# Optimization experiments

Hardware: AMD Instinct MI355X
Metric: run time of the kernel (lower is better)

Reference implementation:

```python
import jax, jax.numpy as jnp
import numpy as np

B_, L_, D_, H_ = 2, 1024, 1024, 16


def _matrixR(L, d_model):
    # Transformer-XL sinusoid table, reversed along the position axis (reverse=True)
    inv_freq = 1.0 / (10000.0 ** (np.arange(0, d_model, 2, dtype=np.float32) / d_model))
    sinus = np.arange(L, dtype=np.float32)[:, None] * inv_freq[None, :]
    mat = np.zeros((L, d_model), dtype=np.float32)
    mat[:, 0::2] = np.sin(sinus)
    mat[:, 1::2] = np.cos(sinus)
    return jnp.asarray(mat[::-1].copy())


def _shift_b(x):
    # x: (b, h, L, L) -> TXL relative shift + lower-triangular mask
    b, h, L, _ = x.shape
    pad = jnp.concatenate([jnp.zeros((b, h, L, 1), x.dtype), x], axis=-1)  # (b,h,L,L+1)
    shifted = pad.reshape(b, h, L + 1, L)[:, :, 1:, :]                      # (b,h,L,L)
    return jnp.tril(shifted)


def setup_inputs() -> dict:
    key = jax.random.key(0)
    ks = jax.random.split(key, 8)
    s = 1.0 / np.sqrt(D_)
    return {
        "E": jax.random.normal(ks[0], (B_, L_, D_), dtype=jnp.float32),
        "Ev": jax.random.normal(ks[1], (B_, L_, D_), dtype=jnp.float32),
        "R": _matrixR(L_, D_),
        "Wq": jax.random.normal(ks[2], (D_, D_), dtype=jnp.float32) * s,
        "Wke": jax.random.normal(ks[3], (D_, D_), dtype=jnp.float32) * s,
        "Wkr": jax.random.normal(ks[4], (D_, D_), dtype=jnp.float32) * s,
        "Wv": jax.random.normal(ks[5], (D_, D_), dtype=jnp.float32) * s,
        "cb": jnp.ones((D_,), dtype=jnp.float32),
        "pb": jnp.ones((D_,), dtype=jnp.float32),
        "Wo_w": jax.random.normal(ks[6], (D_, D_), dtype=jnp.float32) * s,
        "Wo_b": jnp.zeros((D_,), dtype=jnp.float32),
        "ln_g": jnp.ones((D_,), dtype=jnp.float32),
        "ln_b": jnp.zeros((D_,), dtype=jnp.float32),
    }


def reference(E, Ev, R, Wq, Wke, Wkr, Wv, cb, pb, Wo_w, Wo_b, ln_g, ln_b):
    b, L, d = E.shape
    h = H_
    dh = d // h
    # projections -> (b, h, L, dh)
    q = (E @ Wq).reshape(b, L, h, dh).transpose(0, 2, 1, 3)
    k = (Ev @ Wke).reshape(b, L, h, dh).transpose(0, 2, 1, 3)
    v = (Ev @ Wv).reshape(b, L, h, dh).transpose(0, 2, 1, 3)
    # relative-position keys (batch independent): (h, L, dh)
    Q = (R @ Wkr).reshape(L, h, dh).transpose(1, 0, 2)
    # (a) content-content
    A_a = jnp.einsum('bhid,bhjd->bhij', q, k)
    # (b) content-position, with shift trick
    A_b = _shift_b(jnp.einsum('bhid,hjd->bhij', q, Q))
    # (c) global content bias (same for every query row)
    A_c = jnp.einsum('hd,bhjd->bhj', cb.reshape(h, dh), k)[:, :, None, :]  # (b,h,1,L)
    # (d) global position bias (batch independent), shifted
    d_row = jnp.einsum('hd,hjd->hj', pb.reshape(h, dh), Q)                 # (h,L)
    A_d = _shift_b(jnp.broadcast_to(d_row[None, :, None, :], (1, h, L, L)))
    A = A_a + A_b + A_c + A_d
    p = jax.nn.softmax(A, axis=-1)
    Oh = jnp.einsum('bhij,bhjd->bhid', p, v)
    O = Oh.transpose(0, 2, 1, 3).reshape(b, L, d)
    # residual + output proj (dropout is identity in eval) + LayerNorm
    res = Ev + (O @ Wo_w + Wo_b)
    mu = jnp.mean(res, axis=-1, keepdims=True)
    var = jnp.mean((res - mu) ** 2, axis=-1, keepdims=True)
    return (res - mu) * jax.lax.rsqrt(var + 1e-5) * ln_g + ln_b
```

## Files before the change

### kernel.cpp

```cpp
#include <hip/hip_runtime.h>
#include <hip/hip_bf16.h>
#include <math.h>

#define B_ 2
#define L_ 1024
#define D_ 1024
#define H_ 16

typedef short short8 __attribute__((ext_vector_type(8)));
typedef float f32x4  __attribute__((ext_vector_type(4)));

__device__ __forceinline__ short f2bf(float f) {
  unsigned u = __float_as_uint(f);
  u += 0x7fff + ((u >> 16) & 1);
  return (short)(u >> 16);
}
__device__ __forceinline__ float bf2f(short s) {
  return __uint_as_float(((unsigned)(unsigned short)s) << 16);
}
__device__ __forceinline__ int swz(int row, int slot) {
  return row * 64 + ((slot ^ (row & 7)) << 3);
}
__device__ __forceinline__ int vswz(int d, int j) {
  return d * 64 + ((((j >> 3) ^ (d & 7) ^ ((d >> 3) & 7)) & 7) << 3) + (j & 7);
}

__device__ __forceinline__ void glds16(const void* g, void* l) {
  __builtin_amdgcn_global_load_lds((const __attribute__((address_space(1))) void*)g,
                                   (__attribute__((address_space(3))) void*)l, 16, 0, 0);
}

__global__ __launch_bounds__(256) void castbf(
    const float* __restrict__ E, const float* __restrict__ Ev,
    const float* __restrict__ R, short* __restrict__ o) {
  size_t i8 = ((size_t)blockIdx.x * 256 + threadIdx.x) * 8;
  const float* src; size_t off;
  if (i8 < 2097152)      { src = E;  off = i8; }
  else if (i8 < 4194304) { src = Ev; off = i8 - 2097152; }
  else                   { src = R;  off = i8 - 4194304; }
  float4 a = *(const float4*)&src[off];
  float4 b = *(const float4*)&src[off + 4];
  short8 v;
  v[0] = f2bf(a.x); v[1] = f2bf(a.y); v[2] = f2bf(a.z); v[3] = f2bf(a.w);
  v[4] = f2bf(b.x); v[5] = f2bf(b.y); v[6] = f2bf(b.z); v[7] = f2bf(b.w);
  *(short8*)&o[i8] = v;
}

template<int OUT_F32>
__device__ __forceinline__ void mm_glds(const short* __restrict__ A,
                                        const short* __restrict__ Bt,
                                        void* Cp, int N, int K,
                                        int bx, int by) {
  __shared__ short As[8192];
  __shared__ short Bs[8192];
  const int tid = threadIdx.x;
  const int l = tid & 63, w = tid >> 6;
  const int row0 = by * 128, col0 = bx * 128;
  const int wm = (w >> 1) * 64, wn = (w & 1) * 64;
  const f32x4 fz = {0.f, 0.f, 0.f, 0.f};

  f32x4 acc[4][4];
  #pragma unroll
  for (int i = 0; i < 4; ++i)
    #pragma unroll
    for (int j = 0; j < 4; ++j) acc[i][j] = fz;

  const int lrow = l >> 3;
  const int lcol = (l & 7) * 8;

  for (int t = 0; t < K / 64; ++t) {
    const int k0 = t * 64;
    if (t) __syncthreads();
    #pragma unroll
    for (int c = 0; c < 4; ++c) {
      const int rr = (w * 4 + c) * 8 + lrow;
      glds16(&A[(size_t)(row0 + rr) * K + k0 + lcol], &As[(w * 4 + c) * 512]);
      glds16(&Bt[(size_t)(col0 + rr) * K + k0 + lcol], &Bs[(w * 4 + c) * 512]);
    }
    __syncthreads();
    #pragma unroll
    for (int kf = 0; kf < 2; ++kf) {
      short8 a[4], b[4];
      #pragma unroll
      for (int mf = 0; mf < 4; ++mf)
        a[mf] = *(const short8*)&As[(wm + mf * 16 + (l & 15)) * 64 + (kf * 4 + (l >> 4)) * 8];
      #pragma unroll
      for (int nf = 0; nf < 4; ++nf)
        b[nf] = *(const short8*)&Bs[(wn + nf * 16 + (l & 15)) * 64 + (kf * 4 + (l >> 4)) * 8];
      #pragma unroll
      for (int mf = 0; mf < 4; ++mf)
        #pragma unroll
        for (int nf = 0; nf < 4; ++nf)
          acc[mf][nf] = __builtin_amdgcn_mfma_f32_16x16x32_bf16(a[mf], b[nf], acc[mf][nf], 0, 0, 0);
    }
  }

  #pragma unroll
  for (int mf = 0; mf < 4; ++mf)
    #pragma unroll
    for (int nf = 0; nf < 4; ++nf)
      #pragma unroll
      for (int r = 0; r < 4; ++r) {
        int row = row0 + wm + mf * 16 + (l >> 4) * 4 + r;
        int col = col0 + wn + nf * 16 + (l & 15);
        if (OUT_F32) ((float*)Cp)[(size_t)row * N + col] = acc[mf][nf][r];
        else         ((short*)Cp)[(size_t)row * N + col] = f2bf(acc[mf][nf][r]);
      }
}

__global__ __launch_bounds__(256) void proj_mfma(
    const short* __restrict__ Eb, const short* __restrict__ Evb,
    const short* __restrict__ Rb, const short* __restrict__ Wt,
    short* __restrict__ qb, short* __restrict__ kb,
    short* __restrict__ vb, short* __restrict__ Qpb) {
  const int z = blockIdx.z;
  const short* A; const short* Bt; short* C; int M;
  const size_t MM = (size_t)D_ * D_;
  if (z == 0)      { A = Eb;  Bt = Wt;          C = qb;  M = B_ * L_; }
  else if (z == 1) { A = Evb; Bt = Wt + MM;     C = kb;  M = B_ * L_; }
  else if (z == 2) { A = Evb; Bt = Wt + 3 * MM; C = vb;  M = B_ * L_; }
  else             { A = Rb;  Bt = Wt + 2 * MM; C = Qpb; M = L_;      }
  if ((int)blockIdx.y * 128 >= M) return;
  mm_glds<0>(A, Bt, C, D_, D_, blockIdx.x, blockIdx.y);
}

__global__ __launch_bounds__(256) void out_mfma(
    const short* __restrict__ Ob, const short* __restrict__ Wot, float* __restrict__ proj) {
  mm_glds<1>(Ob, Wot, proj, D_, D_, blockIdx.x, blockIdx.y);
}

__global__ __launch_bounds__(256) void tcast(
    const float* __restrict__ W0, const float* __restrict__ W1,
    const float* __restrict__ W2, const float* __restrict__ W3,
    const float* __restrict__ W4, short* __restrict__ out) {
  const int z = blockIdx.z;
  const float* W = (z == 0) ? W0 : (z == 1) ? W1 : (z == 2) ? W2 : (z == 3) ? W3 : W4;
  short* Wt = out + (size_t)z * D_ * D_;
  __shared__ short t[64][65];
  const int tid = threadIdx.x;
  const int r0 = blockIdx.y * 64, c0 = blockIdx.x * 64;
  #pragma unroll
  for (int i = 0; i < 4; ++i) {
    int idx = tid + i * 256;
    int r = idx >> 4, c4 = (idx & 15) * 4;
    float4 v = *(const float4*)&W[(size_t)(r0 + r) * D_ + c0 + c4];
    t[c4 + 0][r] = f2bf(v.x); t[c4 + 1][r] = f2bf(v.y);
    t[c4 + 2][r] = f2bf(v.z); t[c4 + 3][r] = f2bf(v.w);
  }
  __syncthreads();
  #pragma unroll
  for (int i = 0; i < 2; ++i) {
    int idx = tid + i * 256;
    int rr = idx >> 3, cc = (idx & 7) * 8;
    short8 o;
    #pragma unroll
    for (int e = 0; e < 8; ++e) o[e] = t[rr][cc + e];
    *(short8*)&Wt[(size_t)(c0 + rr) * D_ + r0 + cc] = o;
  }
}

__global__ __launch_bounds__(256) void cdvec(
    const short* __restrict__ kb, const short* __restrict__ Qpb,
    const float* __restrict__ cb, const float* __restrict__ pb,
    float* __restrict__ cvec, float* __restrict__ dvec) {
  int idx = blockIdx.x * 256 + threadIdx.x;
  if (idx < B_ * H_ * L_) {
    int b = idx >> 14, h = (idx >> 10) & 15, j = idx & 1023;
    const short* kr = &kb[(size_t)(b * L_ + j) * D_ + h * 64];
    const float* cr = &cb[h * 64];
    float s = 0.f;
    #pragma unroll
    for (int d8 = 0; d8 < 8; ++d8) {
      short8 kv = *(const short8*)&kr[d8 * 8];
      #pragma unroll
      for (int e = 0; e < 8; ++e) s += bf2f(kv[e]) * cr[d8 * 8 + e];
    }
    cvec[idx] = s;
  } else {
    int i2 = idx - B_ * H_ * L_;
    if (i2 < H_ * L_) {
      int h = i2 >> 10, m = i2 & 1023;
      const short* qr = &Qpb[(size_t)m * D_ + h * 64];
      const float* pr = &pb[h * 64];
      float s = 0.f;
      #pragma unroll
      for (int d8 = 0; d8 < 8; ++d8) {
        short8 qv = *(const short8*)&qr[d8 * 8];
        #pragma unroll
        for (int e = 0; e < 8; ++e) s += bf2f(qv[e]) * pr[d8 * 8 + e];
      }
      dvec[i2] = s;
    }
  }
}

__global__ __launch_bounds__(256) void attn_mfma(
    const short* __restrict__ qb, const short* __restrict__ kb,
    const short* __restrict__ vb, const short* __restrict__ Qpb,
    const float* __restrict__ cvec, const float* __restrict__ dvec,
    short* __restrict__ Ob) {
  __shared__ short q_s[4096];
  __shared__ short k_s[4096];
  __shared__ short vt_s[4096];
  __shared__ short win_s[8192];
  __shared__ short pb_s[4 * 1312];
  __shared__ float cvec_s[64];
  __shared__ float dvec_s[128];

  const int tid = threadIdx.x;
  const int l = tid & 63, w = tid >> 6;
  const int nib = L_ / 64;
  const int b  = blockIdx.x / (H_ * nib);
  const int hh = (blockIdx.x / nib) % H_;
  const int i0 = (blockIdx.x % nib) * 64;
  const f32x4 fz = {0.f, 0.f, 0.f, 0.f};
  const short8 sz = {0, 0, 0, 0, 0, 0, 0, 0};

  short8 rk[2], rv[2], rw[4];
  float rc = 0.f, rd = 0.f;

  auto stage_load = [&](int jt) {
    const int j0 = jt * 64;
    const bool pos = (j0 <= i0);
    const int mbase = L_ - 64 - i0 + j0;
    #pragma unroll
    for (int c = 0; c < 2; ++c) {
      int ci = tid + c * 256;
      int r = ci >> 3, s = ci & 7;
      rk[c] = *(const short8*)&kb[(size_t)(b * L_ + j0 + r) * D_ + hh * 64 + s * 8];
      rv[c] = *(const short8*)&vb[(size_t)(b * L_ + j0 + r) * D_ + hh * 64 + s * 8];
    }
    if (pos) {
      #pragma unroll
      for (int c = 0; c < 4; ++c) {
        int ci = tid + c * 256;
        int mm = ci >> 3, s = ci & 7;
        int m = mbase + mm;
        rw[c] = (m < L_) ? *(const short8*)&Qpb[(size_t)m * D_ + hh * 64 + s * 8] : sz;
      }
      if (tid < 128) {
        int m = mbase + tid;
        rd = (m < L_) ? dvec[hh * L_ + m] : 0.f;
      }
    }
    if (tid < 64) rc = cvec[(size_t)(b * H_ + hh) * L_ + j0 + tid];
  };

  auto stage_write = [&](int jt) {
    const bool pos = (jt * 64 <= i0);
    #pragma unroll
    for (int c = 0; c < 2; ++c) {
      int ci = tid + c * 256;
      int r = ci >> 3, s = ci & 7;
      *(short8*)&k_s[swz(r, s)] = rk[c];
      #pragma unroll
      for (int e = 0; e < 8; ++e) {
        int d = s * 8 + e;
        vt_s[vswz(d, r)] = rv[c][e];
      }
    }
    if (pos) {
      #pragma unroll
      for (int c = 0; c < 4; ++c) {
        int ci = tid + c * 256;
        int mm = ci >> 3, s = ci & 7;
        *(short8*)&win_s[swz(mm, s)] = rw[c];
      }
      if (tid < 128) dvec_s[tid] = rd;
    }
    if (tid < 64) cvec_s[tid] = rc;
  };

  short8 rq[2];
  #pragma unroll
  for (int c = 0; c < 2; ++c) {
    int ci = tid + c * 256;
    int r = ci >> 3, s = ci & 7;
    rq[c] = *(const short8*)&qb[(size_t)(b * L_ + i0 + r) * D_ + hh * 64 + s * 8];
  }
  stage_load(0);
  #pragma unroll
  for (int c = 0; c < 2; ++c) {
    int ci = tid + c * 256;
    *(short8*)&q_s[swz(ci >> 3, ci & 7)] = rq[c];
  }
  __syncthreads();

  short8 aq[2];
  {
    int row = w * 16 + (l & 15);
    aq[0] = *(const short8*)&q_s[swz(row, (l >> 4))];
    aq[1] = *(const short8*)&q_s[swz(row, 4 + (l >> 4))];
  }

  float mrow[4], lrow[4];
  f32x4 oacc[4];
  #pragma unroll
  for (int r = 0; r < 4; ++r) { mrow[r] = -3.0e38f; lrow[r] = 0.f; }
  #pragma unroll
  for (int nf = 0; nf < 4; ++nf) oacc[nf] = fz;

  for (int jt = 0; jt < 16; ++jt) {
    const int j0 = jt * 64;
    const bool pos = (j0 <= i0);
    const bool diag = (j0 == i0);

    stage_write(jt);
    __syncthreads();
    if (jt < 15) stage_load(jt + 1);

    f32x4 sac[4];
    #pragma unroll
    for (int nf = 0; nf < 4; ++nf) sac[nf] = fz;
    #pragma unroll
    for (int kf = 0; kf < 2; ++kf) {
      #pragma unroll
      for (int nf = 0; nf < 4; ++nf) {
        short8 bk = *(const short8*)&k_s[swz(nf * 16 + (l & 15), kf * 4 + (l >> 4))];
        sac[nf] = __builtin_amdgcn_mfma_f32_16x16x32_bf16(aq[kf], bk, sac[nf], 0, 0, 0);
      }
    }

    if (pos) {
      f32x4 pacc[5];
      #pragma unroll
      for (int u = 0; u < 5; ++u) pacc[u] = fz;
      const int nf0 = 3 - w;
      #pragma unroll
      for (int kf = 0; kf < 2; ++kf) {
        #pragma unroll
        for (int u = 0; u < 5; ++u) {
          short8 bw = *(const short8*)&win_s[swz((nf0 + u) * 16 + (l & 15), kf * 4 + (l >> 4))];
          pacc[u] = __builtin_amdgcn_mfma_f32_16x16x32_bf16(aq[kf], bw, pacc[u], 0, 0, 0);
        }
      }
      const int pbb = w * 1312;
      #pragma unroll
      for (int u = 0; u < 5; ++u)
        #pragma unroll
        for (int r = 0; r < 4; ++r) {
          int row = (l >> 4) * 4 + r;
          pb_s[pbb + row * 82 + u * 16 + (l & 15)] = f2bf(pacc[u][r]);
        }
    }

    #pragma unroll
    for (int nf = 0; nf < 4; ++nf)
      #pragma unroll
      for (int r = 0; r < 4; ++r) {
        int rj = nf * 16 + (l & 15);
        float s = sac[nf][r] + cvec_s[rj];
        if (pos) {
          int ris = (l >> 4) * 4 + r;
          int rib = w * 16 + ris;
          if (!diag || rj <= rib) {
            s += bf2f(pb_s[w * 1312 + ris * 82 + (15 - ris + rj)]);
            s += dvec_s[63 - rib + rj];
          }
        }
        sac[nf][r] = s;
      }

    #pragma unroll
    for (int r = 0; r < 4; ++r) {
      float mx = fmaxf(fmaxf(sac[0][r], sac[1][r]), fmaxf(sac[2][r], sac[3][r]));
      #pragma unroll
      for (int off = 1; off < 16; off <<= 1)
        mx = fmaxf(mx, __shfl_xor(mx, off, 64));
      float mn = fmaxf(mrow[r], mx);
      float sc = __expf(mrow[r] - mn);
      mrow[r] = mn;
      float ls = 0.f;
      #pragma unroll
      for (int nf = 0; nf < 4; ++nf) {
        float p = __expf(sac[nf][r] - mn);
        sac[nf][r] = p;
        ls += p;
      }
      #pragma unroll
      for (int off = 1; off < 16; off <<= 1)
        ls += __shfl_xor(ls, off, 64);
      lrow[r] = lrow[r] * sc + ls;
      #pragma unroll
      for (int nf = 0; nf < 4; ++nf) oacc[nf][r] *= sc;
    }

    #pragma unroll
    for (int nf = 0; nf < 4; ++nf)
      #pragma unroll
      for (int r = 0; r < 4; ++r) {
        int row = (l >> 4) * 4 + r;
        int col = nf * 16 + (l & 15);
        pb_s[w * 1312 + row * 64 + (((col >> 3) ^ (row & 7)) << 3) + (col & 7)] = f2bf(sac[nf][r]);
      }

    #pragma unroll
    for (int kf = 0; kf < 2; ++kf) {
      int prow = l & 15;
      short8 ap = *(const short8*)&pb_s[w * 1312 + prow * 64 + (((kf * 4 + (l >> 4)) ^ (prow & 7)) << 3)];
      #pragma unroll
      for (int nf = 0; nf < 4; ++nf) {
        short8 bv = *(const short8*)&vt_s[vswz(nf * 16 + (l & 15), (kf * 4 + (l >> 4)) * 8)];
        oacc[nf] = __builtin_amdgcn_mfma_f32_16x16x32_bf16(ap, bv, oacc[nf], 0, 0, 0);
      }
    }
    __syncthreads();
  }

  #pragma unroll
  for (int r = 0; r < 4; ++r) {
    float inv = 1.f / lrow[r];
    #pragma unroll
    for (int nf = 0; nf < 4; ++nf) {
      int row = i0 + w * 16 + (l >> 4) * 4 + r;
      int col = hh * 64 + nf * 16 + (l & 15);
      Ob[(size_t)(b * L_ + row) * D_ + col] = f2bf(oacc[nf][r] * inv);
    }
  }
}

__global__ __launch_bounds__(256) void ln_kernel(
    const float* __restrict__ Ev, const float* __restrict__ proj,
    const float* __restrict__ Wo_b, const float* __restrict__ g,
    const float* __restrict__ beta, float* __restrict__ out) {
  const int row = blockIdx.x;
  __shared__ float red[8];
  const int tid = threadIdx.x;
  const int d = tid * 4;

  float4 e  = *(const float4*)&Ev[(size_t)row * D_ + d];
  float4 p  = *(const float4*)&proj[(size_t)row * D_ + d];
  float4 wb = *(const float4*)&Wo_b[d];
  float4 rr = { e.x + p.x + wb.x, e.y + p.y + wb.y,
                e.z + p.z + wb.z, e.w + p.w + wb.w };
  float sum = rr.x + rr.y + rr.z + rr.w;
  float sq  = rr.x * rr.x + rr.y * rr.y + rr.z * rr.z + rr.w * rr.w;

  #pragma unroll
  for (int off = 1; off < 64; off <<= 1) {
    sum += __shfl_xor(sum, off, 64);
    sq  += __shfl_xor(sq,  off, 64);
  }
  const int wid = tid >> 6;
  if ((tid & 63) == 0) { red[wid * 2] = sum; red[wid * 2 + 1] = sq; }
  __syncthreads();
  sum = red[0] + red[2] + red[4] + red[6];
  sq  = red[1] + red[3] + red[5] + red[7];

  const float mu   = sum * (1.f / (float)D_);
  const float var  = sq * (1.f / (float)D_) - mu * mu;
  const float rstd = rsqrtf(var + 1e-5f);

  float4 gg = *(const float4*)&g[d];
  float4 bb = *(const float4*)&beta[d];
  float4 o = { (rr.x - mu) * rstd * gg.x + bb.x,
               (rr.y - mu) * rstd * gg.y + bb.y,
               (rr.z - mu) * rstd * gg.z + bb.z,
               (rr.w - mu) * rstd * gg.w + bb.w };
  *(float4*)&out[(size_t)row * D_ + d] = o;
}

extern "C" void kernel_launch(void* const* d_in, const int* in_sizes, int n_in,
                              void* d_out, int out_size, void* d_ws, size_t ws_size,
                              hipStream_t stream) {
  const float* E    = (const float*)d_in[0];
  const float* Ev   = (const float*)d_in[1];
  const float* R    = (const float*)d_in[2];
  const float* Wq   = (const float*)d_in[3];
  const float* Wke  = (const float*)d_in[4];
  const float* Wkr  = (const float*)d_in[5];
  const float* Wv   = (const float*)d_in[6];
  const float* cb   = (const float*)d_in[7];
  const float* pb   = (const float*)d_in[8];
  const float* Wo_w = (const float*)d_in[9];
  const float* Wo_b = (const float*)d_in[10];
  const float* ln_g = (const float*)d_in[11];
  const float* ln_b = (const float*)d_in[12];
  float* out = (float*)d_out;

  short* ws   = (short*)d_ws;
  short* Eb   = ws;
  short* Evb  = ws + 2097152;
  short* Rb   = ws + 4194304;
  short* qb   = ws + 5242880;
  short* kb   = ws + 7340032;
  short* vb   = ws + 9437184;
  short* Qpb  = ws + 11534336;
  short* Wt   = ws + 12582912;
  short* Ob   = ws + 17825792;
  float* proj = (float*)Eb;
  float* cvec = (float*)Rb;
  float* dvec = cvec + 32768;

  castbf<<<2560, 256, 0, stream>>>(E, Ev, R, Eb);

  tcast<<<dim3(16, 16, 5), 256, 0, stream>>>(Wq, Wke, Wkr, Wv, Wo_w, Wt);

  proj_mfma<<<dim3(8, 16, 4), 256, 0, stream>>>(Eb, Evb, Rb, Wt, qb, kb, vb, Qpb);

  cdvec<<<192, 256, 0, stream>>>(kb, Qpb, cb, pb, cvec, dvec);

  attn_mfma<<<B_ * H_ * (L_ / 64), 256, 0, stream>>>(qb, kb, vb, Qpb, cvec, dvec, Ob);

  out_mfma<<<dim3(8, 16), 256, 0, stream>>>(Ob, Wt + 4 * (size_t)D_ * D_, proj);

  ln_kernel<<<B_ * L_, 256, 0, stream>>>(Ev, proj, Wo_b, ln_g, ln_b, out);
}
```

Before: 227.0 us.

## Split attention over key halves with combine pass, retile GEMMs, fuse prep kernels

Attention is split into two key-range halves along a second grid dimension. Each half writes unnormalized fp32 partial outputs plus its running max and sum, and a new combine kernel merges the halves into the bf16 output. This doubles the number of attention blocks so more CUs stay busy. The projection and output GEMMs move from 128x128 to 64-row tiles (128 or 64 columns) with an XOR-swizzled LDS layout, giving more blocks and fewer bank conflicts. The activation cast and weight transpose-cast kernels are merged into one launch. MFMA sections are wrapped in s_setprio, and the P-tile swizzle key changes. The cost is an extra kernel plus fp32 partial-output traffic through reused workspace.

```diff
diff --git a/kernel.cpp b/kernel.cpp
--- a/kernel.cpp
+++ b/kernel.cpp
@@ -19,10 +19,13 @@
   return __uint_as_float(((unsigned)(unsigned short)s) << 16);
 }
 __device__ __forceinline__ int swz(int row, int slot) {
-  return row * 64 + ((slot ^ (row & 7)) << 3);
+  return row * 64 + (((slot ^ row) & 7) << 3);
 }
 __device__ __forceinline__ int vswz(int d, int j) {
   return d * 64 + ((((j >> 3) ^ (d & 7) ^ ((d >> 3) & 7)) & 7) << 3) + (j & 7);
+}
+__device__ __forceinline__ int pkey(int row) {
+  return (row & 7) ^ ((row & 8) >> 2);
 }
 
 __device__ __forceinline__ void glds16(const void* g, void* l) {
@@ -30,75 +33,113 @@
                                    (__attribute__((address_space(3))) void*)l, 16, 0, 0);
 }
 
-__global__ __launch_bounds__(256) void castbf(
+__global__ __launch_bounds__(256) void prep(
     const float* __restrict__ E, const float* __restrict__ Ev,
-    const float* __restrict__ R, short* __restrict__ o) {
-  size_t i8 = ((size_t)blockIdx.x * 256 + threadIdx.x) * 8;
-  const float* src; size_t off;
-  if (i8 < 2097152)      { src = E;  off = i8; }
-  else if (i8 < 4194304) { src = Ev; off = i8 - 2097152; }
-  else                   { src = R;  off = i8 - 4194304; }
-  float4 a = *(const float4*)&src[off];
-  float4 b = *(const float4*)&src[off + 4];
-  short8 v;
-  v[0] = f2bf(a.x); v[1] = f2bf(a.y); v[2] = f2bf(a.z); v[3] = f2bf(a.w);
-  v[4] = f2bf(b.x); v[5] = f2bf(b.y); v[6] = f2bf(b.z); v[7] = f2bf(b.w);
-  *(short8*)&o[i8] = v;
-}
-
-template<int OUT_F32>
-__device__ __forceinline__ void mm_glds(const short* __restrict__ A,
-                                        const short* __restrict__ Bt,
-                                        void* Cp, int N, int K,
-                                        int bx, int by) {
-  __shared__ short As[8192];
-  __shared__ short Bs[8192];
+    const float* __restrict__ R,
+    const float* __restrict__ W0, const float* __restrict__ W1,
+    const float* __restrict__ W2, const float* __restrict__ W3,
+    const float* __restrict__ W4,
+    short* __restrict__ act, short* __restrict__ Wt) {
+  __shared__ short t[64][65];
+  const int tid = threadIdx.x;
+  int bid = blockIdx.x;
+  if (bid < 2560) {
+    size_t i8 = ((size_t)bid * 256 + tid) * 8;
+    const float* src; size_t off;
+    if (i8 < 2097152)      { src = E;  off = i8; }
+    else if (i8 < 4194304) { src = Ev; off = i8 - 2097152; }
+    else                   { src = R;  off = i8 - 4194304; }
+    float4 a = *(const float4*)&src[off];
+    float4 b = *(const float4*)&src[off + 4];
+    short8 v;
+    v[0] = f2bf(a.x); v[1] = f2bf(a.y); v[2] = f2bf(a.z); v[3] = f2bf(a.w);
+    v[4] = f2bf(b.x); v[5] = f2bf(b.y); v[6] = f2bf(b.z); v[7] = f2bf(b.w);
+    *(short8*)&act[i8] = v;
+    return;
+  }
+  bid -= 2560;
+  const int z = bid >> 8, rem = bid & 255;
+  const int by = rem >> 4, bx = rem & 15;
+  const float* W = (z == 0) ? W0 : (z == 1) ? W1 : (z == 2) ? W2 : (z == 3) ? W3 : W4;
+  short* Wtz = Wt + (size_t)z * D_ * D_;
+  const int r0 = by * 64, c0 = bx * 64;
+  #pragma unroll
+  for (int i = 0; i < 4; ++i) {
+    int idx = tid + i * 256;
+    int r = idx >> 4, c4 = (idx & 15) * 4;
+    float4 v = *(const float4*)&W[(size_t)(r0 + r) * D_ + c0 + c4];
+    t[c4 + 0][r] = f2bf(v.x); t[c4 + 1][r] = f2bf(v.y);
+    t[c4 + 2][r] = f2bf(v.z); t[c4 + 3][r] = f2bf(v.w);
+  }
+  __syncthreads();
+  #pragma unroll
+  for (int i = 0; i < 2; ++i) {
+    int idx = tid + i * 256;
+    int rr = idx >> 3, cc = (idx & 7) * 8;
+    short8 o;
+    #pragma unroll
+    for (int e = 0; e < 8; ++e) o[e] = t[rr][cc + e];
+    *(short8*)&Wtz[(size_t)(c0 + rr) * D_ + r0 + cc] = o;
+  }
+}
+
+template<int NF, int OUT_F32>
+__device__ __forceinline__ void mm_nf(const short* __restrict__ A,
+                                      const short* __restrict__ Bt,
+                                      void* Cp, int N, int K, int bx, int by) {
+  constexpr int BN = NF * 32;
+  __shared__ short As[4096];
+  __shared__ short Bs[BN * 64];
   const int tid = threadIdx.x;
   const int l = tid & 63, w = tid >> 6;
-  const int row0 = by * 128, col0 = bx * 128;
-  const int wm = (w >> 1) * 64, wn = (w & 1) * 64;
+  const int row0 = by * 64, col0 = bx * BN;
+  const int wm = (w >> 1) * 32, wn = (w & 1) * (NF * 16);
+  const int lr = l >> 3;
+  const int lc = ((l & 7) ^ lr) * 8;
   const f32x4 fz = {0.f, 0.f, 0.f, 0.f};
 
-  f32x4 acc[4][4];
-  #pragma unroll
-  for (int i = 0; i < 4; ++i)
-    #pragma unroll
-    for (int j = 0; j < 4; ++j) acc[i][j] = fz;
-
-  const int lrow = l >> 3;
-  const int lcol = (l & 7) * 8;
+  f32x4 acc[2][NF];
+  #pragma unroll
+  for (int i = 0; i < 2; ++i)
+    #pragma unroll
+    for (int j = 0; j < NF; ++j) acc[i][j] = fz;
 
   for (int t = 0; t < K / 64; ++t) {
     const int k0 = t * 64;
     if (t) __syncthreads();
     #pragma unroll
-    for (int c = 0; c < 4; ++c) {
-      const int rr = (w * 4 + c) * 8 + lrow;
-      glds16(&A[(size_t)(row0 + rr) * K + k0 + lcol], &As[(w * 4 + c) * 512]);
-      glds16(&Bt[(size_t)(col0 + rr) * K + k0 + lcol], &Bs[(w * 4 + c) * 512]);
+    for (int c = 0; c < 2; ++c) {
+      int ch = w * 2 + c;
+      glds16(&A[(size_t)(row0 + ch * 8 + lr) * K + k0 + lc], &As[ch * 512]);
+    }
+    #pragma unroll
+    for (int c = 0; c < NF; ++c) {
+      int ch = w * NF + c;
+      glds16(&Bt[(size_t)(col0 + ch * 8 + lr) * K + k0 + lc], &Bs[ch * 512]);
     }
     __syncthreads();
     #pragma unroll
     for (int kf = 0; kf < 2; ++kf) {
-      short8 a[4], b[4];
-      #pragma unroll
-      for (int mf = 0; mf < 4; ++mf)
-        a[mf] = *(const short8*)&As[(wm + mf * 16 + (l & 15)) * 64 + (kf * 4 + (l >> 4)) * 8];
-      #pragma unroll
-      for (int nf = 0; nf < 4; ++nf)
-        b[nf] = *(const short8*)&Bs[(wn + nf * 16 + (l & 15)) * 64 + (kf * 4 + (l >> 4)) * 8];
-      #pragma unroll
-      for (int mf = 0; mf < 4; ++mf)
+      const int slot = kf * 4 + (l >> 4);
+      short8 a[2], b[NF];
+      #pragma unroll
+      for (int mf = 0; mf < 2; ++mf)
+        a[mf] = *(const short8*)&As[swz(wm + mf * 16 + (l & 15), slot)];
+      #pragma unroll
+      for (int nf = 0; nf < NF; ++nf)
+        b[nf] = *(const short8*)&Bs[swz(wn + nf * 16 + (l & 15), slot)];
+      #pragma unroll
+      for (int mf = 0; mf < 2; ++mf)
         #pragma unroll
-        for (int nf = 0; nf < 4; ++nf)
+        for (int nf = 0; nf < NF; ++nf)
           acc[mf][nf] = __builtin_amdgcn_mfma_f32_16x16x32_bf16(a[mf], b[nf], acc[mf][nf], 0, 0, 0);
     }
   }
 
   #pragma unroll
-  for (int mf = 0; mf < 4; ++mf)
-    #pragma unroll
-    for (int nf = 0; nf < 4; ++nf)
+  for (int mf = 0; mf < 2; ++mf)
+    #pragma unroll
+    for (int nf = 0; nf < NF; ++nf)
       #pragma unroll
       for (int r = 0; r < 4; ++r) {
         int row = row0 + wm + mf * 16 + (l >> 4) * 4 + r;
@@ -120,43 +161,13 @@
   else if (z == 1) { A = Evb; Bt = Wt + MM;     C = kb;  M = B_ * L_; }
   else if (z == 2) { A = Evb; Bt = Wt + 3 * MM; C = vb;  M = B_ * L_; }
   else             { A = Rb;  Bt = Wt + 2 * MM; C = Qpb; M = L_;      }
-  if ((int)blockIdx.y * 128 >= M) return;
-  mm_glds<0>(A, Bt, C, D_, D_, blockIdx.x, blockIdx.y);
+  if ((int)blockIdx.y * 64 >= M) return;
+  mm_nf<4, 0>(A, Bt, C, D_, D_, blockIdx.x, blockIdx.y);
 }
 
 __global__ __launch_bounds__(256) void out_mfma(
     const short* __restrict__ Ob, const short* __restrict__ Wot, float* __restrict__ proj) {
-  mm_glds<1>(Ob, Wot, proj, D_, D_, blockIdx.x, blockIdx.y);
-}
-
-__global__ __launch_bounds__(256) void tcast(
-    const float* __restrict__ W0, const float* __restrict__ W1,
-    const float* __restrict__ W2, const float* __restrict__ W3,
-    const float* __restrict__ W4, short* __restrict__ out) {
-  const int z = blockIdx.z;
-  const float* W = (z == 0) ? W0 : (z == 1) ? W1 : (z == 2) ? W2 : (z == 3) ? W3 : W4;
-  short* Wt = out + (size_t)z * D_ * D_;
-  __shared__ short t[64][65];
-  const int tid = threadIdx.x;
-  const int r0 = blockIdx.y * 64, c0 = blockIdx.x * 64;
-  #pragma unroll
-  for (int i = 0; i < 4; ++i) {
-    int idx = tid + i * 256;
-    int r = idx >> 4, c4 = (idx & 15) * 4;
-    float4 v = *(const float4*)&W[(size_t)(r0 + r) * D_ + c0 + c4];
-    t[c4 + 0][r] = f2bf(v.x); t[c4 + 1][r] = f2bf(v.y);
-    t[c4 + 2][r] = f2bf(v.z); t[c4 + 3][r] = f2bf(v.w);
-  }
-  __syncthreads();
-  #pragma unroll
-  for (int i = 0; i < 2; ++i) {
-    int idx = tid + i * 256;
-    int rr = idx >> 3, cc = (idx & 7) * 8;
-    short8 o;
-    #pragma unroll
-    for (int e = 0; e < 8; ++e) o[e] = t[rr][cc + e];
-    *(short8*)&Wt[(size_t)(c0 + rr) * D_ + r0 + cc] = o;
-  }
+  mm_nf<2, 1>(Ob, Wot, proj, D_, D_, blockIdx.x, blockIdx.y);
 }
 
 __global__ __launch_bounds__(256) void cdvec(
@@ -198,12 +209,11 @@
     const short* __restrict__ qb, const short* __restrict__ kb,
     const short* __restrict__ vb, const short* __restrict__ Qpb,
     const float* __restrict__ cvec, const float* __restrict__ dvec,
-    short* __restrict__ Ob) {
-  __shared__ short q_s[4096];
+    float* __restrict__ O0, float* __restrict__ O1, float* __restrict__ ml) {
   __shared__ short k_s[4096];
   __shared__ short vt_s[4096];
   __shared__ short win_s[8192];
-  __shared__ short pb_s[4 * 1312];
+  __shared__ short pbq_s[5248];
   __shared__ float cvec_s[64];
   __shared__ float dvec_s[128];
 
@@ -213,6 +223,8 @@
   const int b  = blockIdx.x / (H_ * nib);
   const int hh = (blockIdx.x / nib) % H_;
   const int i0 = (blockIdx.x % nib) * 64;
+  const int split = blockIdx.y;
+  const int jt0 = split * 8, jt1 = jt0 + 8;
   const f32x4 fz = {0.f, 0.f, 0.f, 0.f};
   const short8 sz = {0, 0, 0, 0, 0, 0, 0, 0};
 
@@ -275,22 +287,21 @@
   #pragma unroll
   for (int c = 0; c < 2; ++c) {
     int ci = tid + c * 256;
-    int r = ci >> 3, s = ci & 7;
-    rq[c] = *(const short8*)&qb[(size_t)(b * L_ + i0 + r) * D_ + hh * 64 + s * 8];
-  }
-  stage_load(0);
+    rq[c] = *(const short8*)&qb[(size_t)(b * L_ + i0 + (ci >> 3)) * D_ + hh * 64 + (ci & 7) * 8];
+  }
+  stage_load(jt0);
   #pragma unroll
   for (int c = 0; c < 2; ++c) {
     int ci = tid + c * 256;
-    *(short8*)&q_s[swz(ci >> 3, ci & 7)] = rq[c];
+    *(short8*)&pbq_s[swz(ci >> 3, ci & 7)] = rq[c];
   }
   __syncthreads();
 
   short8 aq[2];
   {
     int row = w * 16 + (l & 15);
-    aq[0] = *(const short8*)&q_s[swz(row, (l >> 4))];
-    aq[1] = *(const short8*)&q_s[swz(row, 4 + (l >> 4))];
+    aq[0] = *(const short8*)&pbq_s[swz(row, (l >> 4))];
+    aq[1] = *(const short8*)&pbq_s[swz(row, 4 + (l >> 4))];
   }
 
   float mrow[4], lrow[4];
@@ -300,18 +311,19 @@
   #pragma unroll
   for (int nf = 0; nf < 4; ++nf) oacc[nf] = fz;
 
-  for (int jt = 0; jt < 16; ++jt) {
+  for (int jt = jt0; jt < jt1; ++jt) {
     const int j0 = jt * 64;
     const bool pos = (j0 <= i0);
     const bool diag = (j0 == i0);
 
     stage_write(jt);
     __syncthreads();
-    if (jt < 15) stage_load(jt + 1);
+    if (jt + 1 < jt1) stage_load(jt + 1);
 
     f32x4 sac[4];
     #pragma unroll
     for (int nf = 0; nf < 4; ++nf) sac[nf] = fz;
+    __builtin_amdgcn_s_setprio(1);
     #pragma unroll
     for (int kf = 0; kf < 2; ++kf) {
       #pragma unroll
@@ -320,12 +332,14 @@
         sac[nf] = __builtin_amdgcn_mfma_f32_16x16x32_bf16(aq[kf], bk, sac[nf], 0, 0, 0);
       }
     }
+    __builtin_amdgcn_s_setprio(0);
 
     if (pos) {
       f32x4 pacc[5];
       #pragma unroll
       for (int u = 0; u < 5; ++u) pacc[u] = fz;
       const int nf0 = 3 - w;
+      __builtin_amdgcn_s_setprio(1);
       #pragma unroll
       for (int kf = 0; kf < 2; ++kf) {
         #pragma unroll
@@ -334,13 +348,14 @@
           pacc[u] = __builtin_amdgcn_mfma_f32_16x16x32_bf16(aq[kf], bw, pacc[u], 0, 0, 0);
         }
       }
+      __builtin_amdgcn_s_setprio(0);
       const int pbb = w * 1312;
       #pragma unroll
       for (int u = 0; u < 5; ++u)
         #pragma unroll
         for (int r = 0; r < 4; ++r) {
           int row = (l >> 4) * 4 + r;
-          pb_s[pbb + row * 82 + u * 16 + (l & 15)] = f2bf(pacc[u][r]);
+          pbq_s[pbb + row * 82 + u * 16 + (l & 15)] = f2bf(pacc[u][r]);
         }
     }
 
@@ -354,7 +369,7 @@
           int ris = (l >> 4) * 4 + r;
           int rib = w * 16 + ris;
           if (!diag || rj <= rib) {
-            s += bf2f(pb_s[w * 1312 + ris * 82 + (15 - ris + rj)]);
+            s += bf2f(pbq_s[w * 1312 + ris * 82 + (15 - ris + rj)]);
             s += dvec_s[63 - rib + rj];
           }
         }
@@ -391,32 +406,57 @@
       for (int r = 0; r < 4; ++r) {
         int row = (l >> 4) * 4 + r;
         int col = nf * 16 + (l & 15);
-        pb_s[w * 1312 + row * 64 + (((col >> 3) ^ (row & 7)) << 3) + (col & 7)] = f2bf(sac[nf][r]);
-      }
-
+        pbq_s[w * 1312 + row * 64 + (((col >> 3) ^ pkey(row)) << 3) + (col & 7)] = f2bf(sac[nf][r]);
+      }
+
+    __builtin_amdgcn_s_setprio(1);
     #pragma unroll
     for (int kf = 0; kf < 2; ++kf) {
       int prow = l & 15;
-      short8 ap = *(const short8*)&pb_s[w * 1312 + prow * 64 + (((kf * 4 + (l >> 4)) ^ (prow & 7)) << 3)];
+      short8 ap = *(const short8*)&pbq_s[w * 1312 + prow * 64 + (((kf * 4 + (l >> 4)) ^ pkey(prow)) << 3)];
       #pragma unroll
       for (int nf = 0; nf < 4; ++nf) {
         short8 bv = *(const short8*)&vt_s[vswz(nf * 16 + (l & 15), (kf * 4 + (l >> 4)) * 8)];
         oacc[nf] = __builtin_amdgcn_mfma_f32_16x16x32_bf16(ap, bv, oacc[nf], 0, 0, 0);
       }
     }
+    __builtin_amdgcn_s_setprio(0);
     __syncthreads();
   }
 
+  float* Op = split ? O1 : O0;
   #pragma unroll
   for (int r = 0; r < 4; ++r) {
-    float inv = 1.f / lrow[r];
-    #pragma unroll
-    for (int nf = 0; nf < 4; ++nf) {
-      int row = i0 + w * 16 + (l >> 4) * 4 + r;
-      int col = hh * 64 + nf * 16 + (l & 15);
-      Ob[(size_t)(b * L_ + row) * D_ + col] = f2bf(oacc[nf][r] * inv);
-    }
-  }
+    int ri = (l >> 4) * 4 + r;
+    int row = (b * H_ + hh) * L_ + i0 + w * 16 + ri;
+    #pragma unroll
+    for (int nf = 0; nf < 4; ++nf)
+      Op[(size_t)row * 64 + nf * 16 + (l & 15)] = oacc[nf][r];
+    if ((l & 15) == 0) {
+      ml[split * 65536 + row] = mrow[r];
+      ml[split * 65536 + 32768 + row] = lrow[r];
+    }
+  }
+}
+
+__global__ __launch_bounds__(256) void combine(
+    const float* __restrict__ O0, const float* __restrict__ O1,
+    const float* __restrict__ ml, short* __restrict__ Ob) {
+  int id = blockIdx.x * 256 + threadIdx.x;
+  int row = id >> 3, c8 = (id & 7) * 8;
+  float m0 = ml[row],         l0 = ml[32768 + row];
+  float m1 = ml[65536 + row], l1 = ml[65536 + 32768 + row];
+  float M = fmaxf(m0, m1);
+  float w0 = __expf(m0 - M), w1 = __expf(m1 - M);
+  float inv = 1.f / (w0 * l0 + w1 * l1);
+  const float* p0 = &O0[(size_t)row * 64 + c8];
+  const float* p1 = &O1[(size_t)row * 64 + c8];
+  short8 o;
+  #pragma unroll
+  for (int e = 0; e < 8; ++e)
+    o[e] = f2bf((w0 * p0[e] + w1 * p1[e]) * inv);
+  int b = row >> 14, h = (row >> 10) & 15, i = row & 1023;
+  *(short8*)&Ob[(size_t)(b * L_ + i) * D_ + h * 64 + c8] = o;
 }
 
 __global__ __launch_bounds__(256) void ln_kernel(
@@ -491,18 +531,22 @@
   float* proj = (float*)Eb;
   float* cvec = (float*)Rb;
   float* dvec = cvec + 32768;
-
-  castbf<<<2560, 256, 0, stream>>>(E, Ev, R, Eb);
-
-  tcast<<<dim3(16, 16, 5), 256, 0, stream>>>(Wq, Wke, Wkr, Wv, Wo_w, Wt);
-
-  proj_mfma<<<dim3(8, 16, 4), 256, 0, stream>>>(Eb, Evb, Rb, Wt, qb, kb, vb, Qpb);
+  float* ml   = dvec + 16384;
+  float* O0   = (float*)Eb;
+  float* O1   = (float*)Wt;
+
+  prep<<<3840, 256, 0, stream>>>(E, Ev, R, Wq, Wke, Wkr, Wv, Wo_w, Eb, Wt);
+
+  proj_mfma<<<dim3(8, 32, 4), 256, 0, stream>>>(Eb, Evb, Rb, Wt, qb, kb, vb, Qpb);
 
   cdvec<<<192, 256, 0, stream>>>(kb, Qpb, cb, pb, cvec, dvec);
 
-  attn_mfma<<<B_ * H_ * (L_ / 64), 256, 0, stream>>>(qb, kb, vb, Qpb, cvec, dvec, Ob);
-
-  out_mfma<<<dim3(8, 16), 256, 0, stream>>>(Ob, Wt + 4 * (size_t)D_ * D_, proj);
+  attn_mfma<<<dim3(B_ * H_ * (L_ / 64), 2), 256, 0, stream>>>(
+      qb, kb, vb, Qpb, cvec, dvec, O0, O1, ml);
+
+  combine<<<1024, 256, 0, stream>>>(O0, O1, ml, Ob);
+
+  out_mfma<<<dim3(16, 32), 256, 0, stream>>>(Ob, Wt + 4 * (size_t)D_ * D_, proj);
 
   ln_kernel<<<B_ * L_, 256, 0, stream>>>(Ev, proj, Wo_b, ln_g, ln_b, out);
 }
```

New measurement: 217.6 us. 1.04x faster.
